# Kernel optimization log

Hardware: AMD Instinct MI355X
Metric: run time of the kernel (lower is better)

## Reference

```python
import jax, jax.numpy as jnp
import numpy as np

EPS = 1e-5
RADIUS = 1.0

def bn(x, gamma, beta, axis=1):
    # inference-mode BatchNorm1d: running_mean=0, running_var=1
    shape = [1] * x.ndim
    shape[axis] = -1
    return x * (gamma / jnp.sqrt(1.0 + EPS)).reshape(shape) + beta.reshape(shape)

def pconv(x, w):
    # pointwise Conv1d (kernel_size=1): x [B,Cin,N], w [Cout,Cin]
    return jnp.einsum('oi,bin->bon', w, x)

def sq_dist(a, b):
    # a [B,N,3], b [B,S,3] -> squared pairwise distances [B,N,S]
    return (jnp.sum(a * a, -1)[:, :, None] + jnp.sum(b * b, -1)[:, None, :]
            - 2.0 * jnp.einsum('bnc,bsc->bns', a, b))

def index_points(points, idx):
    # points [B,S,...], idx [B,...] -> gathered [B, idx.shape[1:], ...]
    return jax.vmap(lambda p, i: p[i])(points, idx)

def fps(xyz, npoint):
    # farthest point sampling (deterministic start at index 0)
    B, N, _ = xyz.shape
    binds = jnp.arange(B)
    def step(carry, _):
        dist, far = carry
        c = xyz[binds, far]                                    # [B,3]
        d = jnp.sum((xyz - c[:, None, :]) ** 2, -1)            # [B,N]
        dist = jnp.minimum(dist, d)
        nxt = jnp.argmax(dist, -1).astype(jnp.int32)
        return (dist, nxt), far
    init = (jnp.full((B, N), 1e10, xyz.dtype), jnp.zeros((B,), jnp.int32))
    _, idx = jax.lax.scan(step, init, None, length=npoint)
    return jnp.transpose(idx)                                   # [B,npoint]

def query_ball(radius, nsample, xyz, new_xyz):
    # indices of first nsample points within radius of each center
    B, N, _ = xyz.shape
    S = new_xyz.shape[1]
    d2 = sq_dist(new_xyz, xyz)                                  # [B,S,N]
    gidx = jnp.broadcast_to(jnp.arange(N, dtype=jnp.int32), (B, S, N))
    gidx = jnp.where(d2 > radius * radius, N, gidx)
    gidx = jnp.sort(gidx, axis=-1)[:, :, :nsample]
    first = gidx[:, :, :1]
    gidx = jnp.where(gidx == N, first, gidx)
    return jnp.clip(gidx, 0, N - 1)

def sample_and_group(npoint, nsample, radius, xyz, points):
    fps_idx = fps(xyz, npoint)
    new_xyz = index_points(xyz, fps_idx)                        # [B,S,3]
    new_pts = index_points(points, fps_idx)                     # [B,S,D]
    idx = query_ball(radius, nsample, xyz, new_xyz)             # [B,S,K]
    grouped = index_points(points, idx)                         # [B,S,K,D]
    centered = grouped - new_pts[:, :, None, :]
    rep = jnp.broadcast_to(new_pts[:, :, None, :], centered.shape)
    return new_xyz, jnp.concatenate([centered, rep], axis=-1)   # [B,S,K,2D]

def local_op(x, w1, g1, b1, w2, g2, b2):
    # x [B,n,K,d]; shared pointwise MLP over channels then max over K
    h = jnp.einsum('oi,bnki->bnok', w1, x)
    h = jax.nn.relu(bn(h, g1, b1, axis=2))
    h = jnp.einsum('oi,bnik->bnok', w2, h)
    h = jax.nn.relu(bn(h, g2, b2, axis=2))
    return jnp.transpose(jnp.max(h, -1), (0, 2, 1))             # [B,out,n]

def feature_prop(xyz1, xyz2, points1, points2, w1, g1, b1, w2, g2, b2):
    # 3-NN inverse-distance interpolation of points2 onto xyz1, concat points1
    p1 = jnp.transpose(xyz1, (0, 2, 1))                         # [B,N,3]
    p2 = jnp.transpose(xyz2, (0, 2, 1))                         # [B,S,3]
    f2 = jnp.transpose(points2, (0, 2, 1))                      # [B,S,D2]
    negd, idx = jax.lax.top_k(-sq_dist(p1, p2), 3)              # [B,N,3]
    recip = 1.0 / (-negd + 1e-8)
    w = recip / jnp.sum(recip, -1, keepdims=True)
    interp = jnp.sum(index_points(f2, idx) * w[..., None], 2)   # [B,N,D2]
    new = jnp.concatenate([points1, jnp.transpose(interp, (0, 2, 1))], axis=1)
    new = jax.nn.relu(bn(pconv(new, w1), g1, b1))
    new = jax.nn.relu(bn(pconv(new, w2), g2, b2))
    return new


def setup_inputs() -> dict:
    key = jax.random.key(0)
    ks = iter(jax.random.split(key, 80))
    def W(*s):  return jax.random.normal(next(ks), s, jnp.float32) * 0.05
    def G(n):   return 1.0 + 0.1 * jax.random.normal(next(ks), (n,), jnp.float32)
    def Bt(n):  return 0.1 * jax.random.normal(next(ks), (n,), jnp.float32)
    inp = {"x": jax.random.uniform(next(ks), (4, 8192, 3), jnp.float32)}
    inp.update(w_emb1=W(64, 3), g_emb1=G(64), be_emb1=Bt(64),
               w_emb2=W(64, 64), g_emb2=G(64), be_emb2=Bt(64),
               l0_w1=W(128, 128), l0_g1=G(128), l0_b1=Bt(128),
               l0_w2=W(128, 128), l0_g2=G(128), l0_b2=Bt(128),
               l1_w1=W(256, 256), l1_g1=G(256), l1_b1=Bt(256),
               l1_w2=W(256, 256), l1_g2=G(256), l1_b2=Bt(256),
               f0_w1=W(256, 384), f0_g1=G(256), f0_b1=Bt(256),
               f0_w2=W(512, 256), f0_g2=G(512), f0_b2=Bt(512),
               f1_w1=W(512, 576), f1_g1=G(512), f1_b1=Bt(512),
               f1_w2=W(1024, 512), f1_g2=G(1024), f1_b2=Bt(1024),
               c1_w=W(512, 1024), c1_bias=Bt(512), c1_g=G(512), c1_beta=Bt(512),
               c2_w=W(128, 512), c2_bias=Bt(128), c2_g=G(128), c2_beta=Bt(128),
               out_w=W(8, 128), out_bias=Bt(8))
    return inp


def reference(x, w_emb1, g_emb1, be_emb1, w_emb2, g_emb2, be_emb2,
              l0_w1, l0_g1, l0_b1, l0_w2, l0_g2, l0_b2,
              l1_w1, l1_g1, l1_b1, l1_w2, l1_g2, l1_b2,
              f0_w1, f0_g1, f0_b1, f0_w2, f0_g2, f0_b2,
              f1_w1, f1_g1, f1_b1, f1_w2, f1_g2, f1_b2,
              c1_w, c1_bias, c1_g, c1_beta, c2_w, c2_bias, c2_g, c2_beta,
              out_w, out_bias):
    xyz = x                                                     # [B,N,3]
    h = jnp.transpose(x, (0, 2, 1))                             # [B,3,N]
    h = jax.nn.relu(bn(pconv(h, w_emb1), g_emb1, be_emb1))
    h = jax.nn.relu(bn(pconv(h, w_emb2), g_emb2, be_emb2))
    feats0 = h                                                  # [B,64,N]
    xyz1, g1f = sample_and_group(2048, 32, RADIUS, xyz, jnp.transpose(h, (0, 2, 1)))
    feats1 = local_op(g1f, l0_w1, l0_g1, l0_b1, l0_w2, l0_g2, l0_b2)   # [B,128,2048]
    xyz2, g2f = sample_and_group(1024, 32, RADIUS, xyz1, jnp.transpose(feats1, (0, 2, 1)))
    feats2 = local_op(g2f, l1_w1, l1_g1, l1_b1, l1_w2, l1_g2, l1_b2)   # [B,256,1024]
    h = feature_prop(jnp.transpose(xyz1, (0, 2, 1)), jnp.transpose(xyz2, (0, 2, 1)),
                     feats1, feats2, f0_w1, f0_g1, f0_b1, f0_w2, f0_g2, f0_b2)   # [B,512,2048]
    h = feature_prop(jnp.transpose(xyz, (0, 2, 1)), jnp.transpose(xyz1, (0, 2, 1)),
                     feats0, h, f1_w1, f1_g1, f1_b1, f1_w2, f1_g2, f1_b2)        # [B,1024,N]
    h = jax.nn.relu(bn(pconv(h, c1_w) + c1_bias[None, :, None], c1_g, c1_beta))
    h = jax.nn.relu(bn(pconv(h, c2_w) + c2_bias[None, :, None], c2_g, c2_beta))
    logits = pconv(h, out_w) + out_bias[None, :, None]
    return jnp.transpose(logits, (0, 2, 1))                     # [B,N,labels]
```

## Files before the change

### kernel.cpp

```cpp
#include <hip/hip_runtime.h>
#include <math.h>


static constexpr size_t O_FEATS0 = 0;
static constexpr size_t O_FEATS1 = 8388608;
static constexpr size_t O_FEATS2 = 12582912;
static constexpr size_t O_FP0OUT = 16777216;
static constexpr size_t O_XYZ1   = 33554432;
static constexpr size_t O_XYZ2   = 33652736;
static constexpr size_t O_FPS1   = 33701888;
static constexpr size_t O_FPS2   = 33734656;
static constexpr size_t O_BALL1  = 33751040;
static constexpr size_t O_BALL2  = 34799616;
static constexpr size_t O_NN0I   = 35323904;
static constexpr size_t O_NN0W   = 35422208;
static constexpr size_t O_NN1I   = 35520512;
static constexpr size_t O_NN1W   = 35913728;
static constexpr size_t O_REG0   = 36306944;
static constexpr size_t O_REG1   = 103415808;
static constexpr size_t WS_NEED  = 170524672;

typedef float v2f __attribute__((ext_vector_type(2)));

__global__ __launch_bounds__(256) void emb_kernel(
    const float* __restrict__ xyz, const float* __restrict__ w1,
    const float* __restrict__ g1, const float* __restrict__ b1,
    const float* __restrict__ w2, const float* __restrict__ g2,
    const float* __restrict__ b2, float* __restrict__ out) {
  const int t = threadIdx.x;
  const int o = t & 63, pl = t >> 6;
  const int pt = blockIdx.x * 4 + pl;
  const float x0 = xyz[(size_t)pt * 3 + 0];
  const float x1 = xyz[(size_t)pt * 3 + 1];
  const float x2 = xyz[(size_t)pt * 3 + 2];
  const float SQ = sqrtf(1.0f + 1e-5f);
  float v = w1[o * 3 + 0] * x0 + w1[o * 3 + 1] * x1 + w1[o * 3 + 2] * x2;
  v = fmaxf(v * (g1[o] / SQ) + b1[o], 0.0f);
  __shared__ float h[4][64];
  h[pl][o] = v;
  __syncthreads();
  float acc = 0.0f;
  #pragma unroll 8
  for (int i = 0; i < 64; ++i) acc += w2[o * 64 + i] * h[pl][i];
  float y = fmaxf(acc * (g2[o] / SQ) + b2[o], 0.0f);
  out[(size_t)pt * 64 + o] = y;
}

__device__ __forceinline__ unsigned long long u64max(unsigned long long a,
                                                     unsigned long long b) {
  return a > b ? a : b;
}
template <int CTRL>
__device__ __forceinline__ unsigned long long dpp_step(unsigned long long k) {
  const int lo = (int)(unsigned)k;
  const int hi = (int)(unsigned)(k >> 32);
  const int nlo = __builtin_amdgcn_update_dpp(lo, lo, CTRL, 0xf, 0xf, false);
  const int nhi = __builtin_amdgcn_update_dpp(hi, hi, CTRL, 0xf, 0xf, false);
  return ((unsigned long long)(unsigned)nhi << 32) | (unsigned)nlo;
}

template <int N, int NP>
__global__ __launch_bounds__(512, 1) void fps_kernel(
    const float* __restrict__ xyz, int* __restrict__ out) {
  #pragma clang fp contract(off)
  constexpr int PPT = N / 512;
  constexpr int PAIRS = PPT / 2;
  const int b = blockIdx.x, t = threadIdx.x;
  const float* xb = xyz + (size_t)b * N * 3;
  __shared__ float sx[N], sy[N], sz[N];
  __shared__ unsigned long long skey[2][8];
  for (int i = t; i < N; i += 512) {
    sx[i] = xb[i * 3 + 0];
    sy[i] = xb[i * 3 + 1];
    sz[i] = xb[i * 3 + 2];
  }
  __syncthreads();
  v2f px[PAIRS], py[PAIRS], pz[PAIRS], ds[PAIRS];
  #pragma unroll
  for (int k = 0; k < PAIRS; ++k) {
    const int g = t * PPT + 2 * k;
    px[k].x = sx[g]; px[k].y = sx[g + 1];
    py[k].x = sy[g]; py[k].y = sy[g + 1];
    pz[k].x = sz[g]; pz[k].y = sz[g + 1];
    ds[k].x = 1e10f; ds[k].y = 1e10f;
  }
  const int wid = t >> 6, lane = t & 63;
  int far = 0;
  float ccx = sx[0], ccy = sy[0], ccz = sz[0];
  for (int it = 0; it < NP; ++it) {
    if (t == 0) out[(size_t)b * NP + it] = far;
    v2f cx2, cy2, cz2;
    cx2.x = ccx; cx2.y = ccx;
    cy2.x = ccy; cy2.y = ccy;
    cz2.x = ccz; cz2.y = ccz;
    #pragma unroll
    for (int k = 0; k < PAIRS; ++k) {
      const v2f dx = px[k] - cx2;
      const v2f dy = py[k] - cy2;
      const v2f dz = pz[k] - cz2;
      const v2f d = dx * dx + dy * dy + dz * dz;
      v2f nd;
      nd.x = fminf(ds[k].x, d.x);
      nd.y = fminf(ds[k].y, d.y);
      ds[k] = nd;
    }
    v2f vm = ds[0];
    #pragma unroll
    for (int k = 1; k < PAIRS; ++k) {
      vm.x = fmaxf(vm.x, ds[k].x);
      vm.y = fmaxf(vm.y, ds[k].y);
    }
    const float bv = fmaxf(vm.x, vm.y);
    int bjl = 0;
    #pragma unroll
    for (int k = PAIRS - 1; k >= 0; --k) {
      bjl = (ds[k].y == bv) ? 2 * k + 1 : bjl;
      bjl = (ds[k].x == bv) ? 2 * k : bjl;
    }
    unsigned long long bk =
        ((unsigned long long)__float_as_uint(bv) << 32) |
        (unsigned long long)(unsigned)(~(unsigned)(t * PPT + bjl));
    bk = u64max(bk, dpp_step<0x111>(bk));
    bk = u64max(bk, dpp_step<0x112>(bk));
    bk = u64max(bk, dpp_step<0x114>(bk));
    bk = u64max(bk, dpp_step<0x118>(bk));
    bk = u64max(bk, dpp_step<0x142>(bk));
    bk = u64max(bk, dpp_step<0x143>(bk));
    const int p = it & 1;
    if (lane == 63) skey[p][wid] = bk;
    __syncthreads();
    unsigned long long wk = skey[p][0];
    #pragma unroll
    for (int q = 1; q < 8; ++q) {
      const unsigned long long k2 = skey[p][q];
      wk = (k2 > wk) ? k2 : wk;
    }
    far = (int)(~(unsigned)wk);
    ccx = sx[far]; ccy = sy[far]; ccz = sz[far];
  }
}

__global__ __launch_bounds__(256) void gatherxyz_kernel(
    const float* __restrict__ xyz, const int* __restrict__ idx,
    float* __restrict__ out, int sbits, int N) {
  const int id = blockIdx.x * 256 + threadIdx.x;
  const int b = id >> sbits;
  const int n = idx[id];
  out[(size_t)id * 3 + 0] = xyz[((size_t)b * N + n) * 3 + 0];
  out[(size_t)id * 3 + 1] = xyz[((size_t)b * N + n) * 3 + 1];
  out[(size_t)id * 3 + 2] = xyz[((size_t)b * N + n) * 3 + 2];
}

__global__ __launch_bounds__(256) void ball_kernel(
    const float* __restrict__ xyz, const float* __restrict__ ctr,
    int* __restrict__ out, int sbits, int N) {
  const int t = threadIdx.x;
  const int lane = t & 63, wid = t >> 6;
  const int wg = blockIdx.x * 4 + wid;
  const int b = wg >> sbits;
  __shared__ int lists[4][32];
  const float cx = ctr[(size_t)wg * 3 + 0];
  const float cy = ctr[(size_t)wg * 3 + 1];
  const float cz = ctr[(size_t)wg * 3 + 2];
  const float an = __fadd_rn(__fadd_rn(__fmul_rn(cx, cx), __fmul_rn(cy, cy)),
                             __fmul_rn(cz, cz));
  int fill = 0;
  for (int ch = 0; ch < (N >> 6) && fill < 32; ++ch) {
    const int n = ch * 64 + lane;
    const float bx = xyz[((size_t)b * N + n) * 3 + 0];
    const float by = xyz[((size_t)b * N + n) * 3 + 1];
    const float bz = xyz[((size_t)b * N + n) * 3 + 2];
    const float bb = __fadd_rn(__fadd_rn(__fmul_rn(bx, bx), __fmul_rn(by, by)),
                               __fmul_rn(bz, bz));
    const float dot = __fadd_rn(__fadd_rn(__fmul_rn(cx, bx), __fmul_rn(cy, by)),
                                __fmul_rn(cz, bz));
    const float d2 = __fsub_rn(__fadd_rn(an, bb), __fmul_rn(2.0f, dot));
    const bool q = (d2 <= 1.0f);
    const unsigned long long mask = __ballot(q);
    if (q) {
      const int pos = fill + __popcll(mask & ((1ull << lane) - 1ull));
      if (pos < 32) lists[wid][pos] = n;
    }
    fill += (int)__popcll(mask);
  }
  __syncthreads();
  if (lane < 32) {
    int v = lists[wid][0];
    if (lane < fill) v = lists[wid][lane];
    out[(size_t)wg * 32 + lane] = v;
  }
}

__global__ __launch_bounds__(256) void groupmat_kernel(
    float* __restrict__ Xo, const float* __restrict__ f,
    const int* __restrict__ ball, const int* __restrict__ fps, int g0, int Cf,
    int c4bits, int sbits, int Npts) {
  const int id = blockIdx.x * 256 + threadIdx.x;
  const int c4mask = (1 << c4bits) - 1;
  const int row = id >> c4bits;
  const int col = (id & c4mask) * 4;
  const int gl = g0 + (row >> 5);
  const int k = row & 31;
  const int b = gl >> sbits;
  const int src = ball[(size_t)gl * 32 + k];
  const int ctr = fps[gl];
  const int C = Cf * 2;
  const float* fb = f + (size_t)b * Npts * Cf;
  float4 v;
  if (col < Cf) {
    const float4 a = *(const float4*)(fb + (size_t)src * Cf + col);
    const float4 c = *(const float4*)(fb + (size_t)ctr * Cf + col);
    v = make_float4(a.x - c.x, a.y - c.y, a.z - c.z, a.w - c.w);
  } else {
    v = *(const float4*)(fb + (size_t)ctr * Cf + (col - Cf));
  }
  *(float4*)(Xo + (size_t)row * C + col) = v;
}

#define CMAP(c) ((((c) >> 3) * 12) + ((c) & 7))
__global__ __launch_bounds__(256) void conv_kernel(
    const float* __restrict__ X, const float* __restrict__ W,
    float* __restrict__ Y, int C, int O, const float* __restrict__ gamma,
    const float* __restrict__ beta, const float* __restrict__ bias, int relu) {
  __shared__ float Xs[16][188];
  __shared__ float Ws[16][188];
  const int t = threadIdx.x;
  const size_t m0 = (size_t)blockIdx.x * 128;
  const int o0 = blockIdx.y * 128;
  const int r0 = t >> 2;
  const int cq0 = (t & 3) * 4;
  const int mq = t & 15, nq = t >> 4;
  const int ca = CMAP(r0), cb = CMAP(r0 + 64);
  float acc[8][8];
  #pragma unroll
  for (int i = 0; i < 8; ++i)
    #pragma unroll
    for (int j = 0; j < 8; ++j) acc[i][j] = 0.0f;

  for (int kk = 0; kk < C; kk += 16) {
    const float4 xa = *(const float4*)(X + (m0 + r0) * C + kk + cq0);
    const float4 xb = *(const float4*)(X + (m0 + r0 + 64) * C + kk + cq0);
    const float4 wa = *(const float4*)(W + (size_t)(o0 + r0) * C + kk + cq0);
    const float4 wb = *(const float4*)(W + (size_t)(o0 + r0 + 64) * C + kk + cq0);
    __syncthreads();
    Xs[cq0 + 0][ca] = xa.x; Xs[cq0 + 1][ca] = xa.y;
    Xs[cq0 + 2][ca] = xa.z; Xs[cq0 + 3][ca] = xa.w;
    Xs[cq0 + 0][cb] = xb.x; Xs[cq0 + 1][cb] = xb.y;
    Xs[cq0 + 2][cb] = xb.z; Xs[cq0 + 3][cb] = xb.w;
    Ws[cq0 + 0][ca] = wa.x; Ws[cq0 + 1][ca] = wa.y;
    Ws[cq0 + 2][ca] = wa.z; Ws[cq0 + 3][ca] = wa.w;
    Ws[cq0 + 0][cb] = wb.x; Ws[cq0 + 1][cb] = wb.y;
    Ws[cq0 + 2][cb] = wb.z; Ws[cq0 + 3][cb] = wb.w;
    __syncthreads();
    #pragma unroll
    for (int k = 0; k < 16; ++k) {
      const float4 a0 = *(const float4*)&Xs[k][mq * 12];
      const float4 a1 = *(const float4*)&Xs[k][mq * 12 + 4];
      const float4 b0 = *(const float4*)&Ws[k][nq * 12];
      const float4 b1 = *(const float4*)&Ws[k][nq * 12 + 4];
      const float am[8] = {a0.x, a0.y, a0.z, a0.w, a1.x, a1.y, a1.z, a1.w};
      const float bm[8] = {b0.x, b0.y, b0.z, b0.w, b1.x, b1.y, b1.z, b1.w};
      #pragma unroll
      for (int i = 0; i < 8; ++i)
        #pragma unroll
        for (int j = 0; j < 8; ++j) acc[i][j] += am[i] * bm[j];
    }
  }

  const float SQ = sqrtf(1.0f + 1e-5f);
  float s[8], sh[8];
  #pragma unroll
  for (int j = 0; j < 8; ++j) {
    const int o = o0 + nq * 8 + j;
    const float sc = gamma ? (gamma[o] / SQ) : 1.0f;
    float bb = beta ? beta[o] : 0.0f;
    if (bias) bb = bb + bias[o] * sc;
    s[j] = sc; sh[j] = bb;
  }
  #pragma unroll
  for (int i = 0; i < 8; ++i) {
    float y[8];
    #pragma unroll
    for (int j = 0; j < 8; ++j) {
      float v = acc[i][j] * s[j] + sh[j];
      y[j] = relu ? fmaxf(v, 0.0f) : v;
    }
    const size_t off = (m0 + mq * 8 + i) * O + o0 + nq * 8;
    *(float4*)(Y + off) = make_float4(y[0], y[1], y[2], y[3]);
    *(float4*)(Y + off + 4) = make_float4(y[4], y[5], y[6], y[7]);
  }
}

__global__ __launch_bounds__(256) void segmax_kernel(
    const float* __restrict__ Y, float* __restrict__ F, int O, int obits) {
  const int id = blockIdx.x * 256 + threadIdx.x;
  const int g = id >> obits;
  const int o = id & (O - 1);
  float m = -3.4e38f;
  #pragma unroll 8
  for (int k = 0; k < 32; ++k)
    m = fmaxf(m, Y[((size_t)g * 32 + k) * O + o]);
  F[(size_t)g * O + o] = m;
}

__global__ __launch_bounds__(256) void nn3_kernel(
    const float* __restrict__ txyz, const float* __restrict__ sxyz,
    int* __restrict__ oi, float* __restrict__ ow, int s1bits, int S2) {
  __shared__ float ss[6144];
  const int t = threadIdx.x;
  const int row = blockIdx.x * 256 + t;
  const int b = row >> s1bits;
  for (int i = t; i < S2 * 3; i += 256) ss[i] = sxyz[(size_t)b * S2 * 3 + i];
  __syncthreads();
  const float ax = txyz[(size_t)row * 3 + 0];
  const float ay = txyz[(size_t)row * 3 + 1];
  const float az = txyz[(size_t)row * 3 + 2];
  const float an = __fadd_rn(__fadd_rn(__fmul_rn(ax, ax), __fmul_rn(ay, ay)),
                             __fmul_rn(az, az));
  float d0 = 3.4e38f, d1 = 3.4e38f, d2v = 3.4e38f;
  int i0 = 0, i1 = 0, i2 = 0;
  for (int j = 0; j < S2; ++j) {
    const float bx = ss[j * 3 + 0], by = ss[j * 3 + 1], bz = ss[j * 3 + 2];
    const float bb = __fadd_rn(__fadd_rn(__fmul_rn(bx, bx), __fmul_rn(by, by)),
                               __fmul_rn(bz, bz));
    const float dot = __fadd_rn(__fadd_rn(__fmul_rn(ax, bx), __fmul_rn(ay, by)),
                                __fmul_rn(az, bz));
    const float dd = __fsub_rn(__fadd_rn(an, bb), __fmul_rn(2.0f, dot));
    if (dd < d0) {
      d2v = d1; i2 = i1; d1 = d0; i1 = i0; d0 = dd; i0 = j;
    } else if (dd < d1) {
      d2v = d1; i2 = i1; d1 = dd; i1 = j;
    } else if (dd < d2v) {
      d2v = dd; i2 = j;
    }
  }
  const float r0 = 1.0f / (d0 + 1e-8f);
  const float r1 = 1.0f / (d1 + 1e-8f);
  const float r2 = 1.0f / (d2v + 1e-8f);
  const float sum = __fadd_rn(__fadd_rn(r0, r1), r2);
  oi[(size_t)row * 3 + 0] = i0;
  oi[(size_t)row * 3 + 1] = i1;
  oi[(size_t)row * 3 + 2] = i2;
  ow[(size_t)row * 3 + 0] = r0 / sum;
  ow[(size_t)row * 3 + 1] = r1 / sum;
  ow[(size_t)row * 3 + 2] = r2 / sum;
}

__global__ __launch_bounds__(256) void interp_kernel(
    float* __restrict__ dst, int CT, int c0, const float* __restrict__ src,
    const int* __restrict__ idx, const float* __restrict__ w, int csbits,
    int s1bits, int S2) {
  const int id = blockIdx.x * 256 + threadIdx.x;
  const int row = id >> csbits;
  const int c4 = (id & ((1 << csbits) - 1)) * 4;
  const int Cs = 4 << csbits;
  const int b = row >> s1bits;
  const int j0 = idx[(size_t)row * 3 + 0];
  const int j1 = idx[(size_t)row * 3 + 1];
  const int j2 = idx[(size_t)row * 3 + 2];
  const float w0 = w[(size_t)row * 3 + 0];
  const float w1 = w[(size_t)row * 3 + 1];
  const float w2 = w[(size_t)row * 3 + 2];
  const float4 f0 = *(const float4*)(src + ((size_t)b * S2 + j0) * Cs + c4);
  const float4 f1 = *(const float4*)(src + ((size_t)b * S2 + j1) * Cs + c4);
  const float4 f2 = *(const float4*)(src + ((size_t)b * S2 + j2) * Cs + c4);
  float4 v;
  v.x = f0.x * w0 + f1.x * w1 + f2.x * w2;
  v.y = f0.y * w0 + f1.y * w1 + f2.y * w2;
  v.z = f0.z * w0 + f1.z * w1 + f2.z * w2;
  v.w = f0.w * w0 + f1.w * w1 + f2.w * w2;
  *(float4*)(dst + (size_t)row * CT + c0 + c4) = v;
}

__global__ __launch_bounds__(256) void copycols_kernel(
    float* __restrict__ dst, int CT, int c0, const float* __restrict__ src,
    int csbits) {
  const int id = blockIdx.x * 256 + threadIdx.x;
  const int row = id >> csbits;
  const int c4 = (id & ((1 << csbits) - 1)) * 4;
  const int Cs = 4 << csbits;
  const float4 v = *(const float4*)(src + (size_t)row * Cs + c4);
  *(float4*)(dst + (size_t)row * CT + c0 + c4) = v;
}

__global__ __launch_bounds__(256) void outfinal_kernel(
    const float* __restrict__ X, const float* __restrict__ Wt,
    const float* __restrict__ bias, float* __restrict__ out) {
  __shared__ float Xs[32][132];
  const int t = threadIdx.x;
  const int p0 = blockIdx.x * 32;
  #pragma unroll
  for (int q = 0; q < 4; ++q) {
    const int id = t + q * 256;
    const int r = id >> 5, c4 = (id & 31) * 4;
    const float4 v = *(const float4*)(X + (size_t)(p0 + r) * 128 + c4);
    Xs[r][c4 + 0] = v.x; Xs[r][c4 + 1] = v.y;
    Xs[r][c4 + 2] = v.z; Xs[r][c4 + 3] = v.w;
  }
  __syncthreads();
  const int p = t >> 3, o = t & 7;
  float acc = 0.0f;
  #pragma unroll 8
  for (int i = 0; i < 128; ++i) acc += Wt[o * 128 + i] * Xs[p][i];
  out[(size_t)(p0 + p) * 8 + o] = acc + bias[o];
}

extern "C" void kernel_launch(void* const* d_in, const int* in_sizes, int n_in,
                              void* d_out, int out_size, void* d_ws,
                              size_t ws_size, hipStream_t stream) {
  const float* x       = (const float*)d_in[0];
  const float* w_emb1  = (const float*)d_in[1];
  const float* g_emb1  = (const float*)d_in[2];
  const float* be_emb1 = (const float*)d_in[3];
  const float* w_emb2  = (const float*)d_in[4];
  const float* g_emb2  = (const float*)d_in[5];
  const float* be_emb2 = (const float*)d_in[6];
  const float* l0_w1 = (const float*)d_in[7];
  const float* l0_g1 = (const float*)d_in[8];
  const float* l0_b1 = (const float*)d_in[9];
  const float* l0_w2 = (const float*)d_in[10];
  const float* l0_g2 = (const float*)d_in[11];
  const float* l0_b2 = (const float*)d_in[12];
  const float* l1_w1 = (const float*)d_in[13];
  const float* l1_g1 = (const float*)d_in[14];
  const float* l1_b1 = (const float*)d_in[15];
  const float* l1_w2 = (const float*)d_in[16];
  const float* l1_g2 = (const float*)d_in[17];
  const float* l1_b2 = (const float*)d_in[18];
  const float* f0_w1 = (const float*)d_in[19];
  const float* f0_g1 = (const float*)d_in[20];
  const float* f0_b1 = (const float*)d_in[21];
  const float* f0_w2 = (const float*)d_in[22];
  const float* f0_g2 = (const float*)d_in[23];
  const float* f0_b2 = (const float*)d_in[24];
  const float* f1_w1 = (const float*)d_in[25];
  const float* f1_g1 = (const float*)d_in[26];
  const float* f1_b1 = (const float*)d_in[27];
  const float* f1_w2 = (const float*)d_in[28];
  const float* f1_g2 = (const float*)d_in[29];
  const float* f1_b2 = (const float*)d_in[30];
  const float* c1_w    = (const float*)d_in[31];
  const float* c1_bias = (const float*)d_in[32];
  const float* c1_g    = (const float*)d_in[33];
  const float* c1_beta = (const float*)d_in[34];
  const float* c2_w    = (const float*)d_in[35];
  const float* c2_bias = (const float*)d_in[36];
  const float* c2_g    = (const float*)d_in[37];
  const float* c2_beta = (const float*)d_in[38];
  const float* out_w    = (const float*)d_in[39];
  const float* out_bias = (const float*)d_in[40];

  if (ws_size < WS_NEED) return;

  char* ws = (char*)d_ws;
  float* feats0 = (float*)(ws + O_FEATS0);
  float* feats1 = (float*)(ws + O_FEATS1);
  float* feats2 = (float*)(ws + O_FEATS2);
  float* fp0out = (float*)(ws + O_FP0OUT);
  float* xyz1   = (float*)(ws + O_XYZ1);
  float* xyz2   = (float*)(ws + O_XYZ2);
  int*   fps1   = (int*)(ws + O_FPS1);
  int*   fps2   = (int*)(ws + O_FPS2);
  int*   ball1  = (int*)(ws + O_BALL1);
  int*   ball2  = (int*)(ws + O_BALL2);
  int*   nn0i   = (int*)(ws + O_NN0I);
  float* nn0w   = (float*)(ws + O_NN0W);
  int*   nn1i   = (int*)(ws + O_NN1I);
  float* nn1w   = (float*)(ws + O_NN1W);
  float* REG0   = (float*)(ws + O_REG0);
  float* REG1   = (float*)(ws + O_REG1);
  float* outp   = (float*)d_out;
  hipStream_t s = stream;

  emb_kernel<<<8192, 256, 0, s>>>(x, w_emb1, g_emb1, be_emb1, w_emb2, g_emb2,
                                  be_emb2, feats0);

  fps_kernel<8192, 2048><<<4, 512, 0, s>>>(x, fps1);
  gatherxyz_kernel<<<32, 256, 0, s>>>(x, fps1, xyz1, 11, 8192);
  ball_kernel<<<2048, 256, 0, s>>>(x, xyz1, ball1, 11, 8192);
  for (int c = 0; c < 2; ++c) {
    groupmat_kernel<<<16384, 256, 0, s>>>(REG0, feats0, ball1, fps1, c * 4096,
                                          64, 5, 11, 8192);
    conv_kernel<<<dim3(1024, 1), 256, 0, s>>>(REG0, l0_w1, REG1, 128, 128,
                                              l0_g1, l0_b1, nullptr, 1);
    conv_kernel<<<dim3(1024, 1), 256, 0, s>>>(REG1, l0_w2, REG0, 128, 128,
                                              l0_g2, l0_b2, nullptr, 1);
    segmax_kernel<<<2048, 256, 0, s>>>(REG0, feats1 + (size_t)c * 4096 * 128,
                                       128, 7);
  }

  fps_kernel<2048, 1024><<<4, 512, 0, s>>>(xyz1, fps2);
  gatherxyz_kernel<<<16, 256, 0, s>>>(xyz1, fps2, xyz2, 10, 2048);
  ball_kernel<<<1024, 256, 0, s>>>(xyz1, xyz2, ball2, 10, 2048);
  for (int c = 0; c < 2; ++c) {
    groupmat_kernel<<<16384, 256, 0, s>>>(REG0, feats1, ball2, fps2, c * 2048,
                                          128, 6, 10, 2048);
    conv_kernel<<<dim3(512, 2), 256, 0, s>>>(REG0, l1_w1, REG1, 256, 256,
                                             l1_g1, l1_b1, nullptr, 1);
    conv_kernel<<<dim3(512, 2), 256, 0, s>>>(REG1, l1_w2, REG0, 256, 256,
                                             l1_g2, l1_b2, nullptr, 1);
    segmax_kernel<<<2048, 256, 0, s>>>(REG0, feats2 + (size_t)c * 2048 * 256,
                                       256, 8);
  }

  nn3_kernel<<<32, 256, 0, s>>>(xyz1, xyz2, nn0i, nn0w, 11, 1024);
  copycols_kernel<<<1024, 256, 0, s>>>(REG0, 384, 0, feats1, 5);
  interp_kernel<<<2048, 256, 0, s>>>(REG0, 384, 128, feats2, nn0i, nn0w, 6, 11,
                                     1024);
  conv_kernel<<<dim3(64, 2), 256, 0, s>>>(REG0, f0_w1, REG1, 384, 256, f0_g1,
                                          f0_b1, nullptr, 1);
  conv_kernel<<<dim3(64, 4), 256, 0, s>>>(REG1, f0_w2, fp0out, 256, 512, f0_g2,
                                          f0_b2, nullptr, 1);

  nn3_kernel<<<128, 256, 0, s>>>(x, xyz1, nn1i, nn1w, 13, 2048);
  for (int b = 0; b < 4; b += 2) {
    copycols_kernel<<<1024, 256, 0, s>>>(REG0, 576, 0,
                                         feats0 + (size_t)b * 8192 * 64, 4);
    interp_kernel<<<8192, 256, 0, s>>>(REG0, 576, 64,
                                       fp0out + (size_t)b * 2048 * 512,
                                       nn1i + (size_t)b * 8192 * 3,
                                       nn1w + (size_t)b * 8192 * 3, 7, 13,
                                       2048);
    conv_kernel<<<dim3(128, 4), 256, 0, s>>>(REG0, f1_w1, REG1, 576, 512,
                                             f1_g1, f1_b1, nullptr, 1);
    conv_kernel<<<dim3(128, 8), 256, 0, s>>>(REG1, f1_w2, REG0, 512, 1024,
                                             f1_g2, f1_b2, nullptr, 1);
    conv_kernel<<<dim3(128, 4), 256, 0, s>>>(REG0, c1_w, REG1, 1024, 512,
                                             c1_g, c1_beta, c1_bias, 1);
    conv_kernel<<<dim3(128, 1), 256, 0, s>>>(REG1, c2_w, REG0, 512, 128,
                                             c2_g, c2_beta, c2_bias, 1);
    outfinal_kernel<<<512, 256, 0, s>>>(REG0, out_w, out_bias,
                                        outp + (size_t)b * 8192 * 8);
  }
}
```

Baseline: 5.196 ms.

## Shrink FPS blocks to 256 threads, tree-reduce argmax, fuse xyz gather

The farthest-point-sampling kernel now runs with 256 threads per batch, so each thread holds twice as many points and the cross-wave reduction has only 4 waves per iteration. The per-thread max uses a balanced tree, and the argmax index comes from a bitmask plus count-trailing-zeros instead of a serial select chain. The sampled coordinates are written from shared memory at the end of the kernel, which removes the separate gatherxyz launches. Register pressure per thread doubles (PPT 32 for N=8192), which risks spills or a longer serial distance-update loop on the latency-bound path.

```diff
diff --git a/kernel.cpp b/kernel.cpp
--- a/kernel.cpp
+++ b/kernel.cpp
@@ -60,16 +60,18 @@
 }
 
 template <int N, int NP>
-__global__ __launch_bounds__(512, 1) void fps_kernel(
-    const float* __restrict__ xyz, int* __restrict__ out) {
+__global__ __launch_bounds__(256, 1) void fps_kernel(
+    const float* __restrict__ xyz, int* __restrict__ out,
+    float* __restrict__ oxyz) {
   #pragma clang fp contract(off)
-  constexpr int PPT = N / 512;
+  constexpr int PPT = N / 256;
   constexpr int PAIRS = PPT / 2;
   const int b = blockIdx.x, t = threadIdx.x;
   const float* xb = xyz + (size_t)b * N * 3;
   __shared__ float sx[N], sy[N], sz[N];
-  __shared__ unsigned long long skey[2][8];
-  for (int i = t; i < N; i += 512) {
+  __shared__ int sfar[NP];
+  __shared__ unsigned long long skey[2][4];
+  for (int i = t; i < N; i += 256) {
     sx[i] = xb[i * 3 + 0];
     sy[i] = xb[i * 3 + 1];
     sz[i] = xb[i * 3 + 2];
@@ -88,7 +90,10 @@
   int far = 0;
   float ccx = sx[0], ccy = sy[0], ccz = sz[0];
   for (int it = 0; it < NP; ++it) {
-    if (t == 0) out[(size_t)b * NP + it] = far;
+    if (t == 0) {
+      out[(size_t)b * NP + it] = far;
+      sfar[it] = far;
+    }
     v2f cx2, cy2, cz2;
     cx2.x = ccx; cx2.y = ccx;
     cy2.x = ccy; cy2.y = ccy;
@@ -104,19 +109,28 @@
       nd.y = fminf(ds[k].y, d.y);
       ds[k] = nd;
     }
-    v2f vm = ds[0];
-    #pragma unroll
-    for (int k = 1; k < PAIRS; ++k) {
-      vm.x = fmaxf(vm.x, ds[k].x);
-      vm.y = fmaxf(vm.y, ds[k].y);
-    }
-    const float bv = fmaxf(vm.x, vm.y);
-    int bjl = 0;
-    #pragma unroll
-    for (int k = PAIRS - 1; k >= 0; --k) {
-      bjl = (ds[k].y == bv) ? 2 * k + 1 : bjl;
-      bjl = (ds[k].x == bv) ? 2 * k : bjl;
-    }
+    v2f tv[PAIRS / 2];
+    #pragma unroll
+    for (int k = 0; k < PAIRS / 2; ++k) {
+      tv[k].x = fmaxf(ds[k].x, ds[k + PAIRS / 2].x);
+      tv[k].y = fmaxf(ds[k].y, ds[k + PAIRS / 2].y);
+    }
+    #pragma unroll
+    for (int w = PAIRS / 4; w >= 1; w >>= 1) {
+      #pragma unroll
+      for (int k = 0; k < w; ++k) {
+        tv[k].x = fmaxf(tv[k].x, tv[k + w].x);
+        tv[k].y = fmaxf(tv[k].y, tv[k + w].y);
+      }
+    }
+    const float bv = fmaxf(tv[0].x, tv[0].y);
+    unsigned mask = 0u;
+    #pragma unroll
+    for (int k = 0; k < PAIRS; ++k) {
+      mask |= (ds[k].x == bv) ? (1u << (2 * k)) : 0u;
+      mask |= (ds[k].y == bv) ? (1u << (2 * k + 1)) : 0u;
+    }
+    const int bjl = __builtin_ctz(mask);
     unsigned long long bk =
         ((unsigned long long)__float_as_uint(bv) << 32) |
         (unsigned long long)(unsigned)(~(unsigned)(t * PPT + bjl));
@@ -131,24 +145,20 @@
     __syncthreads();
     unsigned long long wk = skey[p][0];
     #pragma unroll
-    for (int q = 1; q < 8; ++q) {
+    for (int q = 1; q < 4; ++q) {
       const unsigned long long k2 = skey[p][q];
       wk = (k2 > wk) ? k2 : wk;
     }
     far = (int)(~(unsigned)wk);
     ccx = sx[far]; ccy = sy[far]; ccz = sz[far];
   }
-}
-
-__global__ __launch_bounds__(256) void gatherxyz_kernel(
-    const float* __restrict__ xyz, const int* __restrict__ idx,
-    float* __restrict__ out, int sbits, int N) {
-  const int id = blockIdx.x * 256 + threadIdx.x;
-  const int b = id >> sbits;
-  const int n = idx[id];
-  out[(size_t)id * 3 + 0] = xyz[((size_t)b * N + n) * 3 + 0];
-  out[(size_t)id * 3 + 1] = xyz[((size_t)b * N + n) * 3 + 1];
-  out[(size_t)id * 3 + 2] = xyz[((size_t)b * N + n) * 3 + 2];
+  __syncthreads();
+  for (int i = t; i < NP; i += 256) {
+    const int n = sfar[i];
+    oxyz[((size_t)b * NP + i) * 3 + 0] = sx[n];
+    oxyz[((size_t)b * NP + i) * 3 + 1] = sy[n];
+    oxyz[((size_t)b * NP + i) * 3 + 2] = sz[n];
+  }
 }
 
 __global__ __launch_bounds__(256) void ball_kernel(
@@ -475,8 +485,7 @@
   emb_kernel<<<8192, 256, 0, s>>>(x, w_emb1, g_emb1, be_emb1, w_emb2, g_emb2,
                                   be_emb2, feats0);
 
-  fps_kernel<8192, 2048><<<4, 512, 0, s>>>(x, fps1);
-  gatherxyz_kernel<<<32, 256, 0, s>>>(x, fps1, xyz1, 11, 8192);
+  fps_kernel<8192, 2048><<<4, 256, 0, s>>>(x, fps1, xyz1);
   ball_kernel<<<2048, 256, 0, s>>>(x, xyz1, ball1, 11, 8192);
   for (int c = 0; c < 2; ++c) {
     groupmat_kernel<<<16384, 256, 0, s>>>(REG0, feats0, ball1, fps1, c * 4096,
@@ -489,8 +498,7 @@
                                        128, 7);
   }
 
-  fps_kernel<2048, 1024><<<4, 512, 0, s>>>(xyz1, fps2);
-  gatherxyz_kernel<<<16, 256, 0, s>>>(xyz1, fps2, xyz2, 10, 2048);
+  fps_kernel<2048, 1024><<<4, 256, 0, s>>>(xyz1, fps2, xyz2);
   ball_kernel<<<1024, 256, 0, s>>>(xyz1, xyz2, ball2, 10, 2048);
   for (int c = 0; c < 2; ++c) {
     groupmat_kernel<<<16384, 256, 0, s>>>(REG0, feats1, ball2, fps2, c * 2048,
```

After: 5.160 ms. About the same (-0.7%).
